# Performance work log

Hardware: AMD Instinct MI355X
Metric: run time of the kernel (lower is better)

Reference implementation:

```python
import jax, jax.numpy as jnp
import numpy as np

N_USERS = 100000
N_MOVIES = 50000
EMB_DIM = 64
N_EDGES = 5000000


def setup_inputs() -> dict:
    key = jax.random.key(0)
    k1, k2, k3 = jax.random.split(key, 3)
    N = N_USERS + N_MOVIES
    edge_index = jax.random.randint(k1, (2, N_EDGES), 0, N, dtype=jnp.int64)
    user_emb = 0.1 * jax.random.normal(k2, (N_USERS, EMB_DIM), dtype=jnp.float32)
    movie_emb = 0.1 * jax.random.normal(k3, (N_MOVIES, EMB_DIM), dtype=jnp.float32)
    return {"edge_index": edge_index, "n_layers": 3,
            "user_emb": user_emb, "movie_emb": movie_emb}


def reference(edge_index, n_layers, user_emb, movie_emb):
    n_users = user_emb.shape[0]
    N = n_users + movie_emb.shape[0]
    x = jnp.concatenate([user_emb, movie_emb], axis=0)  # [N, D]

    row, col = edge_index[0], edge_index[1]  # source -> target
    # gcn_norm without self-loops (LGConv default): deg from target (col)
    deg = jnp.zeros((N,), x.dtype).at[col].add(1.0)
    dis = jnp.where(deg > 0, jax.lax.rsqrt(jnp.maximum(deg, 1.0)), 0.0)
    norm = dis[row] * dis[col]  # [E]

    acc = x
    total = x
    for _ in range(n_layers):
        msg = acc[row] * norm[:, None]            # [E, D] gather + scale
        acc = jax.ops.segment_sum(msg, col, num_segments=N)  # scatter-add
        total = total + acc
    final = total / (n_layers + 1)                # mean over layers 0..K
    return final[:n_users], final[n_users:]
```

## Files before the change

### kernel.cpp

```cpp
#include <hip/hip_runtime.h>

typedef _Float16 half_t;
typedef _Float16 half2_t __attribute__((ext_vector_type(2)));
union pk_u { unsigned int u; half2_t h; };

#define EMB 64
#define NLAYERS 3
#define BSH2 9
#define BW2 512
#define NB2MAX 512
#define CAP 20480
#define P1_BATCH 4096
#define P1_TH 512
#define P1_EPT 8
#define BINTH 1024

__device__ inline void scan_512w(int* __restrict__ hist, int* __restrict__ lstart,
                                 int* __restrict__ pair) {
    int t = threadIdx.x;
    int a0 = 0, a1 = 0;
    if (t < 256) { a0 = hist[2 * t]; a1 = hist[2 * t + 1]; pair[t] = a0 + a1; }
    __syncthreads();
    for (int off = 1; off < 256; off <<= 1) {
        int u = 0;
        if (t < 256 && t >= off) u = pair[t - off];
        __syncthreads();
        if (t < 256) pair[t] += u;
        __syncthreads();
    }
    if (t < 256) {
        lstart[2 * t]     = pair[t] - a0 - a1;
        lstart[2 * t + 1] = pair[t] - a1;
    }
    __syncthreads();
}

__global__ __launch_bounds__(512) void part_kernel(
        const int* __restrict__ row, const int* __restrict__ col,
        int* __restrict__ gcount, int* __restrict__ tmp, int E, int nb2) {
    __shared__ int hist[NB2MAX];
    __shared__ int lstart[NB2MAX];
    __shared__ int gbase[NB2MAX];
    __shared__ int pair[256];
    __shared__ int srec[P1_BATCH];
    __shared__ unsigned short sbuck[P1_BATCH];

    int base = blockIdx.x * P1_BATCH;
    int nE = min(P1_BATCH, E - base);

    for (int i = threadIdx.x; i < NB2MAX; i += P1_TH) hist[i] = 0;
    __syncthreads();

    int myc[P1_EPT];
    #pragma unroll
    for (int k = 0; k < P1_EPT; ++k) {
        int idx = base + (k << 9) + threadIdx.x;
        int c = (idx < E) ? col[idx] : -1;
        myc[k] = c;
        if (c >= 0) atomicAdd(&hist[c >> BSH2], 1);
    }
    __syncthreads();

    scan_512w(hist, lstart, pair);

    for (int b = threadIdx.x; b < nb2; b += P1_TH) {
        int c = hist[b];
        int off = 0;
        if (c > 0) off = atomicAdd(&gcount[b], c);
        gbase[b] = b * CAP + off - lstart[b];
    }
    __syncthreads();
    for (int b = threadIdx.x; b < NB2MAX; b += P1_TH) hist[b] = lstart[b];
    __syncthreads();

    #pragma unroll
    for (int k = 0; k < P1_EPT; ++k) {
        int idx = base + (k << 9) + threadIdx.x;
        if (idx < E) {
            int c = myc[k];
            int b = c >> BSH2;
            int r = row[idx];
            int pos = atomicAdd(&hist[b], 1);
            srec[pos] = (r << BSH2) | (c & (BW2 - 1));
            sbuck[pos] = (unsigned short)b;
        }
    }
    __syncthreads();

    for (int i = threadIdx.x; i < nE; i += P1_TH)
        tmp[gbase[sbuck[i]] + i] = srec[i];
}

__global__ __launch_bounds__(1024) void bin_kernel(
        const int* __restrict__ tmp, const int* __restrict__ gcount,
        int* __restrict__ eg, int2* __restrict__ sd, float* __restrict__ dis,
        const float4* __restrict__ uev, const float4* __restrict__ mev,
        float4* __restrict__ outv, uint2* __restrict__ s0v,
        int n_users, int N) {
    __shared__ int hist[BW2];
    __shared__ int lstart[BW2];
    __shared__ int pair[256];
    __shared__ float sdis[BW2];
    int b = blockIdx.x;
    int cnt = gcount[b];
    int rbase = b * CAP;
    int c0 = b << BSH2;
    int nc = min(BW2, N - c0);

    for (int i = threadIdx.x; i < BW2; i += BINTH) hist[i] = 0;
    __syncthreads();
    for (int i = threadIdx.x; i < cnt; i += BINTH)
        atomicAdd(&hist[tmp[rbase + i] & (BW2 - 1)], 1);
    __syncthreads();

    scan_512w(hist, lstart, pair);

    for (int c = threadIdx.x; c < nc; c += BINTH) {
        int d = hist[c];
        float dn = (d > 0) ? rsqrtf((float)d) : 0.0f;
        sd[c0 + c] = make_int2(rbase + lstart[c], d);
        dis[c0 + c] = dn;
        sdis[c] = dn;
    }
    __syncthreads();
    for (int i = threadIdx.x; i < BW2; i += BINTH) hist[i] = lstart[i];
    __syncthreads();

    for (int i = threadIdx.x; i < cnt; i += BINTH) {
        int v = tmp[rbase + i];
        int pos = atomicAdd(&hist[v & (BW2 - 1)], 1);
        eg[rbase + pos] = (v >> BSH2) << 4;
    }

    for (int i = threadIdx.x; i < nc * 16; i += BINTH) {
        int loc = i >> 4;
        int node = c0 + loc;
        int q = i & 15;
        const float4* src = (node < n_users) ? (uev + (long long)node * 16)
                                             : (mev + (long long)(node - n_users) * 16);
        float4 v = src[q];
        outv[(long long)node * 16 + q] = v;
        float dn = sdis[loc];
        pk_u w0, w1;
        w0.h[0] = (half_t)(v.x * dn); w0.h[1] = (half_t)(v.y * dn);
        w1.h[0] = (half_t)(v.z * dn); w1.h[1] = (half_t)(v.w * dn);
        s0v[(long long)node * 16 + q] = make_uint2(w0.u, w1.u);
    }
}

template <bool LAST>
__global__ __launch_bounds__(256) void gather_kernel(
        const int* __restrict__ eg, const int2* __restrict__ sd,
        const float* __restrict__ dis,
        const uint2* __restrict__ tab, uint2* __restrict__ sB,
        float4* __restrict__ outv, float scale, int N) {
    int wave = blockIdx.x * (blockDim.x >> 6) + (threadIdx.x >> 6);
    if (wave >= N) return;
    int l = threadIdx.x & 63;
    int p = l & 15;
    int h = l >> 4;
    unsigned pb = (unsigned)p << 3;
    const char* tb = (const char*)tab;

    int2 se = sd[wave];
    int j = se.x;
    int e = se.x + se.y;
    pk_u a01, a23;
    a01.u = 0; a23.u = 0;

    for (; j < e; j += 32) {
        int last = e - 1;
        int r[8];
        bool ok[8];
        #pragma unroll
        for (int k = 0; k < 8; ++k) {
            int idx = j + (k << 2) + h;
            ok[k] = idx < e;
            r[k] = eg[min(idx, last)];
        }
        #pragma unroll
        for (int k = 0; k < 8; ++k) {
            uint2 v = *(const uint2*)(tb + ((unsigned)(r[k] << 3) + pb));
            pk_u t;
            t.u = ok[k] ? v.x : 0u; a01.h += t.h;
            t.u = ok[k] ? v.y : 0u; a23.h += t.h;
        }
    }

    pk_u t;
    t.u = (unsigned int)__shfl_xor((int)a01.u, 16); a01.h += t.h;
    t.u = (unsigned int)__shfl_xor((int)a01.u, 32); a01.h += t.h;
    t.u = (unsigned int)__shfl_xor((int)a23.u, 16); a23.h += t.h;
    t.u = (unsigned int)__shfl_xor((int)a23.u, 32); a23.h += t.h;

    if (h == 0) {
        float dc = dis[wave];
        float g0 = dc * (float)a01.h[0];
        float g1 = dc * (float)a01.h[1];
        float g2 = dc * (float)a23.h[0];
        float g3 = dc * (float)a23.h[1];
        long long o = (long long)wave * 16 + p;
        float4 v = outv[o];
        v.x = (v.x + g0) * scale;
        v.y = (v.y + g1) * scale;
        v.z = (v.z + g2) * scale;
        v.w = (v.w + g3) * scale;
        outv[o] = v;
        if (!LAST) {
            pk_u w0, w1;
            w0.h[0] = (half_t)(dc * g0); w0.h[1] = (half_t)(dc * g1);
            w1.h[0] = (half_t)(dc * g2); w1.h[1] = (half_t)(dc * g3);
            sB[o] = make_uint2(w0.u, w1.u);
        }
    }
}

extern "C" void kernel_launch(void* const* d_in, const int* in_sizes, int n_in,
                              void* d_out, int out_size, void* d_ws, size_t ws_size,
                              hipStream_t stream) {
    const int*   edge = (const int*)d_in[0];
    const float* ue   = (const float*)d_in[2];
    const float* me   = (const float*)d_in[3];
    float*       out  = (float*)d_out;

    const int E        = in_sizes[0] / 2;
    const int n_users  = in_sizes[2] / EMB;
    const int n_movies = in_sizes[3] / EMB;
    const int N        = n_users + n_movies;
    const int* row = edge;
    const int* col = edge + E;
    const int nb2 = (N + BW2 - 1) >> BSH2;

    char* ws = (char*)d_ws;
    auto align_up = [](size_t v) { return (v + 255) & ~(size_t)255; };
    int*    gcount = (int*)ws;    ws += align_up((size_t)NB2MAX * sizeof(int));
    int2*   sd     = (int2*)ws;   ws += align_up((size_t)N * sizeof(int2));
    float*  dis    = (float*)ws;  ws += align_up((size_t)N * sizeof(float));
    int*    tmp    = (int*)ws;    ws += align_up((size_t)nb2 * CAP * sizeof(int));
    int*    eg     = (int*)ws;    ws += align_up((size_t)nb2 * CAP * sizeof(int));
    half_t* sA     = (half_t*)ws; ws += align_up((size_t)N * EMB * sizeof(half_t));
    half_t* sB     = (half_t*)ws; ws += align_up((size_t)N * EMB * sizeof(half_t));

    hipMemsetAsync(gcount, 0, (size_t)NB2MAX * sizeof(int), stream);
    part_kernel<<<(E + P1_BATCH - 1) / P1_BATCH, P1_TH, 0, stream>>>(
        row, col, gcount, tmp, E, nb2);
    bin_kernel<<<nb2, BINTH, 0, stream>>>(
        tmp, gcount, eg, sd, dis,
        (const float4*)ue, (const float4*)me, (float4*)out, (uint2*)sA,
        n_users, N);

    const int waves_per_block = 4;
    const int gblocks = (N + waves_per_block - 1) / waves_per_block;
    gather_kernel<false><<<gblocks, 256, 0, stream>>>(
        eg, sd, dis, (const uint2*)sA, (uint2*)sB, (float4*)out, 1.0f, N);
    gather_kernel<false><<<gblocks, 256, 0, stream>>>(
        eg, sd, dis, (const uint2*)sB, (uint2*)sA, (float4*)out, 1.0f, N);
    gather_kernel<true><<<gblocks, 256, 0, stream>>>(
        eg, sd, dis, (const uint2*)sA, (uint2*)sB, (float4*)out,
        1.0f / (NLAYERS + 1), N);
}
```

Baseline: 497.9 us.

## Pad per-node edge lists to 32 with sentinel, widen gathers to 16B, prefetch indices

The binning kernel now pads each destination node's edge list to a multiple of 32 and fills the padding with a sentinel index that points to a zeroed extra row in the half-precision tables. This removes the per-element bounds checks and selects in the gather loop. The gather kernel switches from 8-byte to 16-byte loads per lane (8 lanes per row, 8 rows in flight) and software-prefetches the next batch of edge indices. The cost is extra padded edge storage and wasted loads for low-degree nodes, since average degree is about 33 and padding can nearly double the work.

```diff
diff --git a/kernel.cpp b/kernel.cpp
--- a/kernel.cpp
+++ b/kernel.cpp
@@ -10,16 +10,17 @@
 #define BW2 512
 #define NB2MAX 512
 #define CAP 20480
+#define EGCAP 28672
 #define P1_BATCH 4096
 #define P1_TH 512
 #define P1_EPT 8
 #define BINTH 1024
 
-__device__ inline void scan_512w(int* __restrict__ hist, int* __restrict__ lstart,
+__device__ inline void scan_512w(const int* __restrict__ in, int* __restrict__ lstart,
                                  int* __restrict__ pair) {
     int t = threadIdx.x;
     int a0 = 0, a1 = 0;
-    if (t < 256) { a0 = hist[2 * t]; a1 = hist[2 * t + 1]; pair[t] = a0 + a1; }
+    if (t < 256) { a0 = in[2 * t]; a1 = in[2 * t + 1]; pair[t] = a0 + a1; }
     __syncthreads();
     for (int off = 1; off < 256; off <<= 1) {
         int u = 0;
@@ -98,14 +99,17 @@
         float4* __restrict__ outv, uint2* __restrict__ s0v,
         int n_users, int N) {
     __shared__ int hist[BW2];
+    __shared__ int padh[BW2];
     __shared__ int lstart[BW2];
     __shared__ int pair[256];
     __shared__ float sdis[BW2];
     int b = blockIdx.x;
     int cnt = gcount[b];
     int rbase = b * CAP;
+    int ebase = b * EGCAP;
     int c0 = b << BSH2;
     int nc = min(BW2, N - c0);
+    int sent = N << 4;
 
     for (int i = threadIdx.x; i < BW2; i += BINTH) hist[i] = 0;
     __syncthreads();
@@ -113,12 +117,16 @@
         atomicAdd(&hist[tmp[rbase + i] & (BW2 - 1)], 1);
     __syncthreads();
 
-    scan_512w(hist, lstart, pair);
+    for (int c = threadIdx.x; c < BW2; c += BINTH)
+        padh[c] = (hist[c] + 31) & ~31;
+    __syncthreads();
+
+    scan_512w(padh, lstart, pair);
 
     for (int c = threadIdx.x; c < nc; c += BINTH) {
         int d = hist[c];
         float dn = (d > 0) ? rsqrtf((float)d) : 0.0f;
-        sd[c0 + c] = make_int2(rbase + lstart[c], d);
+        sd[c0 + c] = make_int2(ebase + lstart[c], padh[c]);
         dis[c0 + c] = dn;
         sdis[c] = dn;
     }
@@ -129,8 +137,19 @@
     for (int i = threadIdx.x; i < cnt; i += BINTH) {
         int v = tmp[rbase + i];
         int pos = atomicAdd(&hist[v & (BW2 - 1)], 1);
-        eg[rbase + pos] = (v >> BSH2) << 4;
-    }
+        eg[ebase + pos] = (v >> BSH2) << 4;
+    }
+    __syncthreads();
+
+    for (int i = threadIdx.x; i < BW2 * 32; i += BINTH) {
+        int c = i >> 5;
+        int o = i & 31;
+        int st = hist[c];
+        int en = lstart[c] + padh[c];
+        if (st + o < en) eg[ebase + st + o] = sent;
+    }
+    int tot = lstart[BW2 - 1] + padh[BW2 - 1];
+    if (threadIdx.x < 64) eg[ebase + tot + threadIdx.x] = sent;
 
     for (int i = threadIdx.x; i < nc * 16; i += BINTH) {
         int loc = i >> 4;
@@ -152,54 +171,67 @@
 __global__ __launch_bounds__(256) void gather_kernel(
         const int* __restrict__ eg, const int2* __restrict__ sd,
         const float* __restrict__ dis,
-        const uint2* __restrict__ tab, uint2* __restrict__ sB,
+        const uint4* __restrict__ tab, uint2* __restrict__ sB,
         float4* __restrict__ outv, float scale, int N) {
     int wave = blockIdx.x * (blockDim.x >> 6) + (threadIdx.x >> 6);
     if (wave >= N) return;
     int l = threadIdx.x & 63;
-    int p = l & 15;
-    int h = l >> 4;
-    unsigned pb = (unsigned)p << 3;
+    int p = l & 7;
+    int h = l >> 3;
+    unsigned pb = (unsigned)p << 4;
     const char* tb = (const char*)tab;
 
     int2 se = sd[wave];
     int j = se.x;
     int e = se.x + se.y;
-    pk_u a01, a23;
-    a01.u = 0; a23.u = 0;
-
-    for (; j < e; j += 32) {
-        int last = e - 1;
-        int r[8];
-        bool ok[8];
-        #pragma unroll
-        for (int k = 0; k < 8; ++k) {
-            int idx = j + (k << 2) + h;
-            ok[k] = idx < e;
-            r[k] = eg[min(idx, last)];
+    pk_u a0, a1, a2, a3;
+    a0.u = 0; a1.u = 0; a2.u = 0; a3.u = 0;
+
+    if (j < e) {
+        int r0 = eg[j + h];
+        int r1 = eg[j + 8 + h];
+        int r2 = eg[j + 16 + h];
+        int r3 = eg[j + 24 + h];
+        for (; j < e; j += 32) {
+            int n0 = eg[j + 32 + h];
+            int n1 = eg[j + 40 + h];
+            int n2 = eg[j + 48 + h];
+            int n3 = eg[j + 56 + h];
+            uint4 v0 = *(const uint4*)(tb + ((unsigned)(r0 << 3) + pb));
+            uint4 v1 = *(const uint4*)(tb + ((unsigned)(r1 << 3) + pb));
+            uint4 v2 = *(const uint4*)(tb + ((unsigned)(r2 << 3) + pb));
+            uint4 v3 = *(const uint4*)(tb + ((unsigned)(r3 << 3) + pb));
+            pk_u t;
+            t.u = v0.x; a0.h += t.h; t.u = v0.y; a1.h += t.h;
+            t.u = v0.z; a2.h += t.h; t.u = v0.w; a3.h += t.h;
+            t.u = v1.x; a0.h += t.h; t.u = v1.y; a1.h += t.h;
+            t.u = v1.z; a2.h += t.h; t.u = v1.w; a3.h += t.h;
+            t.u = v2.x; a0.h += t.h; t.u = v2.y; a1.h += t.h;
+            t.u = v2.z; a2.h += t.h; t.u = v2.w; a3.h += t.h;
+            t.u = v3.x; a0.h += t.h; t.u = v3.y; a1.h += t.h;
+            t.u = v3.z; a2.h += t.h; t.u = v3.w; a3.h += t.h;
+            r0 = n0; r1 = n1; r2 = n2; r3 = n3;
         }
-        #pragma unroll
-        for (int k = 0; k < 8; ++k) {
-            uint2 v = *(const uint2*)(tb + ((unsigned)(r[k] << 3) + pb));
-            pk_u t;
-            t.u = ok[k] ? v.x : 0u; a01.h += t.h;
-            t.u = ok[k] ? v.y : 0u; a23.h += t.h;
-        }
-    }
-
-    pk_u t;
-    t.u = (unsigned int)__shfl_xor((int)a01.u, 16); a01.h += t.h;
-    t.u = (unsigned int)__shfl_xor((int)a01.u, 32); a01.h += t.h;
-    t.u = (unsigned int)__shfl_xor((int)a23.u, 16); a23.h += t.h;
-    t.u = (unsigned int)__shfl_xor((int)a23.u, 32); a23.h += t.h;
-
-    if (h == 0) {
+    }
+
+    #pragma unroll
+    for (int m = 8; m <= 32; m <<= 1) {
+        pk_u t;
+        t.u = (unsigned int)__shfl_xor((int)a0.u, m); a0.h += t.h;
+        t.u = (unsigned int)__shfl_xor((int)a1.u, m); a1.h += t.h;
+        t.u = (unsigned int)__shfl_xor((int)a2.u, m); a2.h += t.h;
+        t.u = (unsigned int)__shfl_xor((int)a3.u, m); a3.h += t.h;
+    }
+
+    if (h < 2) {
+        pk_u x0 = h ? a2 : a0;
+        pk_u x1 = h ? a3 : a1;
         float dc = dis[wave];
-        float g0 = dc * (float)a01.h[0];
-        float g1 = dc * (float)a01.h[1];
-        float g2 = dc * (float)a23.h[0];
-        float g3 = dc * (float)a23.h[1];
-        long long o = (long long)wave * 16 + p;
+        float g0 = dc * (float)x0.h[0];
+        float g1 = dc * (float)x0.h[1];
+        float g2 = dc * (float)x1.h[0];
+        float g3 = dc * (float)x1.h[1];
+        long long o = (long long)wave * 16 + p * 2 + h;
         float4 v = outv[o];
         v.x = (v.x + g0) * scale;
         v.y = (v.y + g1) * scale;
@@ -237,11 +269,13 @@
     int2*   sd     = (int2*)ws;   ws += align_up((size_t)N * sizeof(int2));
     float*  dis    = (float*)ws;  ws += align_up((size_t)N * sizeof(float));
     int*    tmp    = (int*)ws;    ws += align_up((size_t)nb2 * CAP * sizeof(int));
-    int*    eg     = (int*)ws;    ws += align_up((size_t)nb2 * CAP * sizeof(int));
-    half_t* sA     = (half_t*)ws; ws += align_up((size_t)N * EMB * sizeof(half_t));
-    half_t* sB     = (half_t*)ws; ws += align_up((size_t)N * EMB * sizeof(half_t));
+    int*    eg     = (int*)ws;    ws += align_up((size_t)nb2 * EGCAP * sizeof(int));
+    half_t* sA     = (half_t*)ws; ws += align_up((size_t)(N + 1) * EMB * sizeof(half_t));
+    half_t* sB     = (half_t*)ws; ws += align_up((size_t)(N + 1) * EMB * sizeof(half_t));
 
     hipMemsetAsync(gcount, 0, (size_t)NB2MAX * sizeof(int), stream);
+    hipMemsetAsync(sA + (size_t)N * EMB, 0, EMB * sizeof(half_t), stream);
+    hipMemsetAsync(sB + (size_t)N * EMB, 0, EMB * sizeof(half_t), stream);
     part_kernel<<<(E + P1_BATCH - 1) / P1_BATCH, P1_TH, 0, stream>>>(
         row, col, gcount, tmp, E, nb2);
     bin_kernel<<<nb2, BINTH, 0, stream>>>(
@@ -252,10 +286,10 @@
     const int waves_per_block = 4;
     const int gblocks = (N + waves_per_block - 1) / waves_per_block;
     gather_kernel<false><<<gblocks, 256, 0, stream>>>(
-        eg, sd, dis, (const uint2*)sA, (uint2*)sB, (float4*)out, 1.0f, N);
+        eg, sd, dis, (const uint4*)sA, (uint2*)sB, (float4*)out, 1.0f, N);
     gather_kernel<false><<<gblocks, 256, 0, stream>>>(
-        eg, sd, dis, (const uint2*)sB, (uint2*)sA, (float4*)out, 1.0f, N);
+        eg, sd, dis, (const uint4*)sB, (uint2*)sA, (float4*)out, 1.0f, N);
     gather_kernel<true><<<gblocks, 256, 0, stream>>>(
-        eg, sd, dis, (const uint2*)sA, (uint2*)sB, (float4*)out,
+        eg, sd, dis, (const uint4*)sA, (uint2*)sB, (float4*)out,
         1.0f / (NLAYERS + 1), N);
 }
```

Result: no change. 492.9 us (-1.0%).
